# Kernel tuning notes

Hardware: AMD Instinct MI355X
Metric: run time of the kernel (lower is better)

The kernel has to match this reference:

```python
import jax, jax.numpy as jnp
import numpy as np

N, CIN, C, G, K, H, W = 2, 256, 512, 8, 3, 48, 48
CG = C // G          # channels per group (head dim) = 64
PAD = K // 2
HD, WD = H - K + 1, W - K + 1   # k/v spatial grid (pad=False convs)


def _conv(x, w, groups, pad):
    return jax.lax.conv_general_dilated(
        x, w, window_strides=(1, 1), padding=[(pad, pad), (pad, pad)],
        dimension_numbers=('NCHW', 'OIHW', 'NCHW'), feature_group_count=groups)


def setup_inputs() -> dict:
    key = jax.random.key(0)
    ks = jax.random.split(key, 32)

    def wgt(k, shape):
        fan_in = int(np.prod(shape[1:]))
        return jax.random.normal(k, shape, dtype=jnp.float32) * (fan_in ** -0.5)

    inp = {
        'x_in': jax.random.normal(ks[0], (N, CIN, H, W), dtype=jnp.float32),
        'h':    jax.random.normal(ks[1], (N, C, H, W), dtype=jnp.float32),
        'c':    jax.random.normal(ks[2], (N, C, H, W), dtype=jnp.float32),
        'tau':  jnp.full((G,), CG ** -0.5, dtype=jnp.float32),  # init (channels/groups)^-0.5
        # proj_x: 1x1 from input + intergroup 1x1 on h (groups > 1)
        'W_x':  wgt(ks[3], (C, CIN, 1, 1)),
        'W_ig': wgt(ks[4], (C, C, 1, 1)),
        # grouped KxK q/k/v projections on xh (2C channels, G groups)
        'W_q':  wgt(ks[5], (C, 2 * CG, K, K)),
        'W_k':  wgt(ks[6], (C, 2 * CG, K, K)),
        'W_v':  wgt(ks[7], (C, 2 * CG, K, K)),
    }
    for idx, gate in enumerate(['i', 'f', 'g', 'o']):
        inp[f'W{gate}_a'] = wgt(ks[8 + 3 * idx], (C, CG, 1, 1))        # grouped 1x1 on a
        inp[f'W{gate}_x'] = wgt(ks[9 + 3 * idx], (C, 2 * CG, K, K))    # grouped KxK on xh
        inp[f'b_{gate}'] = jnp.zeros((C,), dtype=jnp.float32)
    return inp


def reference(x_in, h, c, tau, W_x, W_ig, W_q, W_k, W_v,
              Wi_a, Wi_x, b_i, Wf_a, Wf_x, b_f,
              Wg_a, Wg_x, b_g, Wo_a, Wo_x, b_o):
    n = x_in.shape[0]
    # proj_x: sum of 1x1 conv branches (input + intergroup h), no bias
    x = _conv(x_in, W_x, 1, 0) + _conv(h, W_ig, 1, 0)          # [n, C, H, W]

    # xh: per-group interleave of x and h -> [n, 2C, H, W]
    xg = x.reshape(n, G, CG, H, W)
    hg = h.reshape(n, G, CG, H, W)
    xh = jnp.stack([xg, hg], axis=2).reshape(n, 2 * C, H, W)
    # dropout is identity in eval

    q = _conv(xh, W_q, G, PAD).reshape(n, G, CG, H * W)         # [n,G,Cg,Q]
    k = _conv(xh, W_k, G, 0).reshape(n, G, CG, HD * WD)         # [n,G,Cg,D]
    v = _conv(xh, W_v, G, 0).reshape(n, G, CG, HD * WD)

    logits = jnp.einsum('g,ngcq,ngcd->ngqd', tau, q, k)
    w = jax.nn.softmax(logits, axis=3)                          # [n,G,Q,D]
    a = jnp.einsum('ngcd,ngqd->ngcq', v, w).reshape(n, C, H, W)

    def gate(Wa, Wx, b):
        return _conv(a, Wa, G, 0) + _conv(xh, Wx, G, PAD) + b[None, :, None, None]

    i = jax.nn.sigmoid(gate(Wi_a, Wi_x, b_i))
    f = jax.nn.sigmoid(gate(Wf_a, Wf_x, b_f))
    g = jnp.tanh(gate(Wg_a, Wg_x, b_g))
    o = jax.nn.sigmoid(gate(Wo_a, Wo_x, b_o))

    c_new = f * c + i * g
    h_new = o * jnp.tanh(c_new)
    return h_new
```

## Files before the change

kernel.cpp:

```cpp
#include <hip/hip_runtime.h>
#include <hip/hip_bf16.h>
#include <math.h>

#define NB   2
#define CIN  256
#define CC   512
#define GG   8
#define CGR  64
#define HH   48
#define WW   48
#define PP   (HH*WW)
#define HD   46
#define WD   46
#define DD   (HD*WD)
#define DPADV 2120
#define WRT  589824

typedef __bf16 bf16x8 __attribute__((ext_vector_type(8)));
typedef float  f32x4  __attribute__((ext_vector_type(4)));

__device__ __forceinline__ bf16x8 ldb8(const __hip_bfloat16* p) {
    return *reinterpret_cast<const bf16x8*>(p);
}
__device__ __forceinline__ void store4bf(__hip_bfloat16* p, f32x4 v) {
    union { __hip_bfloat16 h[4]; uint2 u; } t;
    #pragma unroll
    for (int r = 0; r < 4; ++r) t.h[r] = (__hip_bfloat16)v[r];
    *reinterpret_cast<uint2*>(p) = t.u;
}
__device__ __forceinline__ float ex2(float x) {
    return __builtin_amdgcn_exp2f(x);
}
__device__ __forceinline__ float sig_fast(float x) {
    return __builtin_amdgcn_rcpf(1.f + ex2(-1.44269504088896f * x));
}
__device__ __forceinline__ float tanh_fast(float x) {
    return 1.f - 2.f * __builtin_amdgcn_rcpf(ex2(2.88539008177793f * x) + 1.f);
}

__global__ __launch_bounds__(256) void prep_kernel(
    const float* __restrict__ Wq, const float* __restrict__ Wk,
    const float* __restrict__ Wv, const float* __restrict__ Wix,
    const float* __restrict__ Wfx, const float* __restrict__ Wgx,
    const float* __restrict__ Wox, const float* __restrict__ Wia,
    const float* __restrict__ Wfa, const float* __restrict__ Wga,
    const float* __restrict__ Woa, const float* __restrict__ Wx,
    const float* __restrict__ Wig,
    __hip_bfloat16* __restrict__ Wr, __hip_bfloat16* __restrict__ Wa,
    __hip_bfloat16* __restrict__ Wp)
{
    const int i = blockIdx.x * 256 + threadIdx.x;
    const int N1 = 7 * WRT;
    const int N2 = N1 + 4 * 32768;
    if (i < N1) {
        const int t = i / WRT, r = i % WRT;
        const int g = r / 73728, r2 = r % 73728;
        const int chunk = r2 / 2048, r3 = r2 % 2048;
        const int och = r3 / 32, k = r3 % 32;
        const int tap = chunk >> 2;
        const int ci = (chunk & 3) * 32 + k;
        const int co = g * 64 + och;
        const float* src;
        switch (t) {
            case 0: src = Wq;  break;  case 1: src = Wk;  break;
            case 2: src = Wv;  break;  case 3: src = Wix; break;
            case 4: src = Wfx; break;  case 5: src = Wgx; break;
            default: src = Wox;
        }
        Wr[i] = (__hip_bfloat16)src[(size_t)co * 1152 + ci * 9 + tap];
    } else if (i < N2) {
        const int j = i - N1;
        const int t = j / 32768, r = j % 32768;
        const float* src = (t == 0) ? Wia : (t == 1) ? Wfa : (t == 2) ? Wga : Woa;
        Wa[j] = (__hip_bfloat16)src[r];
    } else {
        const int j = i - N2;
        const int g = j / 49152, r = j % 49152;
        const int chunk = r / 2048, r3 = r % 2048;
        const int och = r3 / 32, k = r3 % 32;
        const int c = g * 64 + och;
        const int ci = chunk * 32 + k;
        Wp[j] = (__hip_bfloat16)((ci < 256) ? Wx[(size_t)c * 256 + ci]
                                            : Wig[(size_t)c * 512 + (ci - 256)]);
    }
}

__global__ __launch_bounds__(256) void xpose_kernel(
    const float* __restrict__ x_in, const float* __restrict__ h,
    __hip_bfloat16* __restrict__ xiT, __hip_bfloat16* __restrict__ xhT)
{
    const int pt = blockIdx.x;
    const int n  = blockIdx.y;
    const int p0 = pt * 16;
    const int tid = threadIdx.x;

    __shared__ float xs[CIN * 17];
    __shared__ float hs[CC * 17];

    const float* xb = x_in + (size_t)n * CIN * PP;
    const float* hb = h + (size_t)n * CC * PP;
    #pragma unroll
    for (int k = 0; k < 16; ++k) {
        const int idx = k * 256 + tid;
        xs[(idx >> 4) * 17 + (idx & 15)] = xb[(size_t)(idx >> 4) * PP + p0 + (idx & 15)];
    }
    #pragma unroll
    for (int k = 0; k < 32; ++k) {
        const int idx = k * 256 + tid;
        hs[(idx >> 4) * 17 + (idx & 15)] = hb[(size_t)(idx >> 4) * PP + p0 + (idx & 15)];
    }
    __syncthreads();

    #pragma unroll
    for (int it = 0; it < 2; ++it) {
        const int u = it * 256 + tid;
        const int pix = u & 15, ck = u >> 4;
        union { __hip_bfloat16 h8[8]; bf16x8 v; } t;
        #pragma unroll
        for (int j = 0; j < 8; ++j)
            t.h8[j] = (__hip_bfloat16)xs[(ck * 8 + j) * 17 + pix];
        *reinterpret_cast<bf16x8*>(
            xiT + ((size_t)n * PP + p0 + pix) * 256 + ck * 8) = t.v;
    }
    #pragma unroll
    for (int it = 0; it < 4; ++it) {
        const int u = it * 256 + tid;
        const int pix = u & 15, ck = u >> 4;
        const int g = ck >> 3, c8 = (ck & 7) * 8;
        union { __hip_bfloat16 h8[8]; bf16x8 v; } t;
        #pragma unroll
        for (int j = 0; j < 8; ++j)
            t.h8[j] = (__hip_bfloat16)hs[(ck * 8 + j) * 17 + pix];
        *reinterpret_cast<bf16x8*>(
            xhT + ((size_t)(n * GG + g) * PP + p0 + pix) * 128 + 64 + c8) = t.v;
    }
}

__global__ __launch_bounds__(256) void proj_mfma_kernel(
    const __hip_bfloat16* __restrict__ xiT, const __hip_bfloat16* __restrict__ Wp,
    __hip_bfloat16* xhT)
{
    const int b = blockIdx.x;
    const int g = b & 7;
    const int j = b >> 3;
    const int n = j / 12;
    const int yt = j % 12;
    const int ng = n * GG + g;
    const int tid = threadIdx.x;
    const int w = tid >> 6, lane = tid & 63;
    const int col = lane & 15, quad = lane >> 4;
    const int y = yt * 4 + w;

    f32x4 acc[12];
    #pragma unroll
    for (int i = 0; i < 12; ++i) acc[i] = (f32x4){0.f, 0.f, 0.f, 0.f};

    const __hip_bfloat16* wgbase = Wp + (size_t)g * 24 * 2048 + col * 32 + quad * 8;

    for (int kk = 0; kk < 24; ++kk) {
        bf16x8 bfr[3];
        if (kk < 8) {
            const __hip_bfloat16* bp =
                xiT + ((size_t)n * PP + y * 48 + col) * 256 + kk * 32 + quad * 8;
            #pragma unroll
            for (int nf = 0; nf < 3; ++nf)
                bfr[nf] = ldb8(bp + (size_t)(nf * 16) * 256);
        } else {
            const int kh = kk - 8;
            const int gp = kh >> 1;
            const int c0 = (kh & 1) * 32;
            const __hip_bfloat16* bp =
                xhT + ((size_t)(n * GG + gp) * PP + y * 48 + col) * 128 + 64 + c0 + quad * 8;
            #pragma unroll
            for (int nf = 0; nf < 3; ++nf)
                bfr[nf] = ldb8(bp + (size_t)(nf * 16) * 128);
        }
        const __hip_bfloat16* wp = wgbase + kk * 2048;
        #pragma unroll
        for (int cf = 0; cf < 4; ++cf) {
            const bf16x8 af = ldb8(wp + cf * 512);
            #pragma unroll
            for (int nf = 0; nf < 3; ++nf)
                acc[cf * 3 + nf] = __builtin_amdgcn_mfma_f32_16x16x32_bf16(
                    af, bfr[nf], acc[cf * 3 + nf], 0, 0, 0);
        }
    }

    __hip_bfloat16* dst = xhT + (size_t)ng * PP * 128;
    #pragma unroll
    for (int cf = 0; cf < 4; ++cf)
        #pragma unroll
        for (int nf = 0; nf < 3; ++nf) {
            const int pix = y * 48 + nf * 16 + col;
            store4bf(dst + (size_t)pix * 128 + cf * 16 + quad * 4, acc[cf * 3 + nf]);
        }
}

__global__ __launch_bounds__(512) void conv_qkv_kernel(
    const __hip_bfloat16* __restrict__ xhT, const __hip_bfloat16* __restrict__ Wr,
    const float* __restrict__ tau,
    __hip_bfloat16* __restrict__ qT, __hip_bfloat16* __restrict__ kT,
    __hip_bfloat16* __restrict__ v)
{
    const int b = blockIdx.x;
    const int xcd = b & 7;
    const int j = b >> 3;
    const int s = xcd + 8 * (j / 12);
    const int yt = j % 12;
    const int t = s / 16;
    const int ng = s % 16;
    const int g = ng & 7;
    const int tid = threadIdx.x;
    const int w8 = tid >> 6, lane = tid & 63;
    const int yw = w8 & 3, chalf = w8 >> 2;
    const int cf0 = chalf * 2;
    const int col = lane & 15, quad = lane >> 4;
    const int y0 = yt * 4;
    const int yy = y0 + yw;
    const int ohw = (t == 0) ? 48 : 46;
    const int d0 = (t == 0) ? -1 : 0;
    const int soff = (t == 0) ? 1 : 0;
    const bool wave_active = (yy < ohw);

    __shared__ __hip_bfloat16 st[8 * 300 * 8];

    const __hip_bfloat16* slab = xhT + (size_t)ng * PP * 128;
    const __hip_bfloat16* wgbase =
        Wr + ((size_t)t * 8 + g) * 36 * 2048 + col * 32 + quad * 8;

    if (tid < 96) {
        const int ck = tid / 12, r2 = tid % 12;
        const int lr = r2 >> 1, side = r2 & 1;
        const int sc = side ? 49 : (soff ? 0 : 48);
        *reinterpret_cast<bf16x8*>(st + ((ck * 300) + lr * 50 + sc) * 8) =
            (bf16x8)(__bf16)0.f;
    }

    f32x4 acc[6];
    #pragma unroll
    for (int i = 0; i < 6; ++i) acc[i] = (f32x4){0.f, 0.f, 0.f, 0.f};

    for (int hc = 0; hc < 2; ++hc) {
        __syncthreads();
        #pragma unroll
        for (int it = 0; it < 5; ++it) {
            const int u = it * 512 + tid;
            if (u < 2304) {
                const int lr = u / 384;
                const int rem = u % 384;
                const int px = rem >> 3, ck = rem & 7;
                const int ry = y0 + d0 + lr;
                const int ryc = max(0, min(47, ry));
                bf16x8 vv = ldb8(slab + ((size_t)(ryc * 48 + px)) * 128 + hc * 64 + ck * 8);
                *reinterpret_cast<bf16x8*>(st + ((ck * 300) + lr * 50 + px + soff) * 8) =
                    (ry == ryc) ? vv : (bf16x8)(__bf16)0.f;
            }
        }
        __syncthreads();
        if (!wave_active) continue;

        #pragma unroll
        for (int ky = 0; ky < 3; ++ky) {
            const int lrk = (yw + ky) * 50;
            #pragma unroll
            for (int kx = 0; kx < 3; ++kx) {
                const int scb = col + kx;
                #pragma unroll
                for (int c32 = 0; c32 < 2; ++c32) {
                    bf16x8 bfr[3];
                    #pragma unroll
                    for (int nf = 0; nf < 3; ++nf)
                        bfr[nf] = *reinterpret_cast<const bf16x8*>(
                            st + (((c32 * 4 + quad) * 300) + lrk + nf * 16 + scb) * 8);
                    const __hip_bfloat16* wp =
                        wgbase + ((ky * 3 + kx) * 4 + hc * 2 + c32) * 2048;
                    if (t != 2) {
                        #pragma unroll
                        for (int cc = 0; cc < 2; ++cc) {
                            const bf16x8 af = ldb8(wp + (cf0 + cc) * 512);
                            #pragma unroll
                            for (int nf = 0; nf < 3; ++nf)
                                acc[cc * 3 + nf] = __builtin_amdgcn_mfma_f32_16x16x32_bf16(
                                    af, bfr[nf], acc[cc * 3 + nf], 0, 0, 0);
                        }
                    } else {
                        #pragma unroll
                        for (int cc = 0; cc < 2; ++cc) {
                            const bf16x8 af = ldb8(wp + (cf0 + cc) * 512);
                            #pragma unroll
                            for (int nf = 0; nf < 3; ++nf)
                                acc[cc * 3 + nf] = __builtin_amdgcn_mfma_f32_16x16x32_bf16(
                                    bfr[nf], af, acc[cc * 3 + nf], 0, 0, 0);
                        }
                    }
                }
            }
        }
    }

    if (!wave_active) return;
    if (t == 0) {
        const float ts = tau[g] * 1.44269504088896340736f;
        __hip_bfloat16* dst = qT + (size_t)ng * PP * 64;
        #pragma unroll
        for (int cc = 0; cc < 2; ++cc)
            #pragma unroll
            for (int nf = 0; nf < 3; ++nf) {
                const int pix = yy * 48 + nf * 16 + col;
                store4bf(dst + (size_t)pix * 64 + (cf0 + cc) * 16 + quad * 4,
                         acc[cc * 3 + nf] * ts);
            }
    } else if (t == 1) {
        __hip_bfloat16* dst = kT + (size_t)ng * DD * 64;
        #pragma unroll
        for (int cc = 0; cc < 2; ++cc)
            #pragma unroll
            for (int nf = 0; nf < 3; ++nf) {
                const int x = nf * 16 + col;
                if (x < 46) {
                    const int pix = yy * 46 + x;
                    store4bf(dst + (size_t)pix * 64 + (cf0 + cc) * 16 + quad * 4,
                             acc[cc * 3 + nf]);
                }
            }
    } else {
        __hip_bfloat16* dst = v + (size_t)ng * 64 * DPADV;
        #pragma unroll
        for (int cc = 0; cc < 2; ++cc) {
            const int co = (cf0 + cc) * 16 + col;
            #pragma unroll
            for (int nf = 0; nf < 3; ++nf) {
                const int x4 = nf * 16 + quad * 4;
                #pragma unroll
                for (int r = 0; r < 4; ++r) {
                    if (x4 + r < 46)
                        dst[(size_t)co * DPADV + yy * 46 + x4 + r] =
                            (__hip_bfloat16)acc[cc * 3 + nf][r];
                }
            }
        }
    }
}

__global__ __launch_bounds__(256) void attn_kernel(
    __hip_bfloat16* qa,
    const __hip_bfloat16* __restrict__ kT,
    const __hip_bfloat16* __restrict__ vT)
{
    const int idx = blockIdx.x;
    const int j3  = idx >> 3;
    const int sub = (j3 >= 144) ? 1 : 0;
    const int ng  = (idx & 7) + 8 * sub;
    const int qt  = j3 - 144 * sub;
    const int tid = threadIdx.x;
    const int w = tid >> 6, lane = tid & 63;
    const int col = lane & 15, quad = lane >> 4;
    const int qbase = qt * 16;

    const int it0 = w * 17;
    const int it1 = (w < 3) ? (it0 + 17) : 66;

    __shared__ float lmS[3][64];
    __shared__ float llS[3][64];
    __shared__ float laccS[3][64][16];

    __hip_bfloat16* qrow = qa + ((size_t)ng * PP + qbase + col) * CGR;
    const bf16x8 qf0 = ldb8(qrow + quad * 8);
    const bf16x8 qf1 = ldb8(qrow + 32 + quad * 8);

    const __hip_bfloat16* kbase = kT + (size_t)ng * DD * CGR;
    const __hip_bfloat16* vbase = vT + (size_t)ng * CGR * DPADV;
    const __hip_bfloat16* vrow[4];
    #pragma unroll
    for (int cf = 0; cf < 4; ++cf)
        vrow[cf] = vbase + (size_t)(cf * 16 + col) * DPADV;

    const int key0 = ((col >> 2) << 3) + (col & 3);
    const __hip_bfloat16* p0 = kbase + (size_t)(it0 * 32 + key0) * CGR + quad * 8;
    const __hip_bfloat16* p1 = p0 + 4 * CGR;

    f32x4 acc[4];
    #pragma unroll
    for (int cf = 0; cf < 4; ++cf) acc[cf] = (f32x4){0.f, 0.f, 0.f, 0.f};
    float m = -INFINITY;
    float l = 0.f;
    const f32x4 zero = {0.f, 0.f, 0.f, 0.f};

    bf16x8 A0 = ldb8(p0), A1 = ldb8(p0 + 32);
    bf16x8 B0 = ldb8(p1), B1 = ldb8(p1 + 32);

    for (int it = it0; it < it1; ++it) {
        const int dbase = it * 32;
        p0 += 32 * CGR; p1 += 32 * CGR;
        bf16x8 nA0, nA1, nB0, nB1;
        if (it + 1 < it1) {
            nA0 = ldb8(p0); nA1 = ldb8(p0 + 32);
            nB0 = ldb8(p1); nB1 = ldb8(p1 + 32);
        }

        f32x4 S0 = __builtin_amdgcn_mfma_f32_16x16x32_bf16(A0, qf0, zero, 0, 0, 0);
        S0 = __builtin_amdgcn_mfma_f32_16x16x32_bf16(A1, qf1, S0, 0, 0, 0);
        f32x4 S1 = __builtin_amdgcn_mfma_f32_16x16x32_bf16(B0, qf0, zero, 0, 0, 0);
        S1 = __builtin_amdgcn_mfma_f32_16x16x32_bf16(B1, qf1, S1, 0, 0, 0);

        const int da = dbase + quad * 8;
        const bf16x8 vf0 = ldb8(vrow[0] + da);
        const bf16x8 vf1 = ldb8(vrow[1] + da);
        const bf16x8 vf2 = ldb8(vrow[2] + da);
        const bf16x8 vf3 = ldb8(vrow[3] + da);

        const float lmx = fmaxf(fmaxf(fmaxf(S0[0], S0[1]), fmaxf(S0[2], S0[3])),
                                fmaxf(fmaxf(S1[0], S1[1]), fmaxf(S1[2], S1[3])));

        if (__any(lmx > m + 8.f)) {
            float s = lmx;
            s = fmaxf(s, __shfl_xor(s, 16, 64));
            s = fmaxf(s, __shfl_xor(s, 32, 64));
            const float mn = fmaxf(m, s);
            const float a = ex2(m - mn);
            l *= a;
            #pragma unroll
            for (int cf = 0; cf < 4; ++cf) acc[cf] *= a;
            m = mn;
        }

        float e[8];
        float lsum = 0.f;
        #pragma unroll
        for (int r = 0; r < 4; ++r) {
            e[r]     = ex2(S0[r] - m);
            e[4 + r] = ex2(S1[r] - m);
            lsum += e[r] + e[4 + r];
        }
        l += lsum;

        bf16x8 pt;
        #pragma unroll
        for (int jj = 0; jj < 8; ++jj) pt[jj] = (__bf16)e[jj];

        acc[0] = __builtin_amdgcn_mfma_f32_16x16x32_bf16(vf0, pt, acc[0], 0, 0, 0);
        acc[1] = __builtin_amdgcn_mfma_f32_16x16x32_bf16(vf1, pt, acc[1], 0, 0, 0);
        acc[2] = __builtin_amdgcn_mfma_f32_16x16x32_bf16(vf2, pt, acc[2], 0, 0, 0);
        acc[3] = __builtin_amdgcn_mfma_f32_16x16x32_bf16(vf3, pt, acc[3], 0, 0, 0);

        A0 = nA0; A1 = nA1; B0 = nB0; B1 = nB1;
    }

    if (w == 3) {
        const int dbase = 66 * 32;
        const int kk0 = min(dbase + key0, DD - 1);
        const int kk1 = min(dbase + key0 + 4, DD - 1);
        const __hip_bfloat16* t0 = kbase + (size_t)kk0 * CGR + quad * 8;
        const __hip_bfloat16* t1 = kbase + (size_t)kk1 * CGR + quad * 8;
        f32x4 S0 = __builtin_amdgcn_mfma_f32_16x16x32_bf16(ldb8(t0), qf0, zero, 0, 0, 0);
        S0 = __builtin_amdgcn_mfma_f32_16x16x32_bf16(ldb8(t0 + 32), qf1, S0, 0, 0, 0);
        f32x4 S1 = __builtin_amdgcn_mfma_f32_16x16x32_bf16(ldb8(t1), qf0, zero, 0, 0, 0);
        S1 = __builtin_amdgcn_mfma_f32_16x16x32_bf16(ldb8(t1 + 32), qf1, S1, 0, 0, 0);

        float e[8];
        #pragma unroll
        for (int r = 0; r < 4; ++r) {
            e[r]     = (dbase + quad * 8 + r     < DD) ? S0[r] : -1e30f;
            e[4 + r] = (dbase + quad * 8 + 4 + r < DD) ? S1[r] : -1e30f;
        }
        float s = fmaxf(fmaxf(fmaxf(e[0], e[1]), fmaxf(e[2], e[3])),
                        fmaxf(fmaxf(e[4], e[5]), fmaxf(e[6], e[7])));
        s = fmaxf(s, __shfl_xor(s, 16, 64));
        s = fmaxf(s, __shfl_xor(s, 32, 64));
        const float mn = fmaxf(m, s);
        const float a = ex2(m - mn);
        float lsum = 0.f;
        #pragma unroll
        for (int jj = 0; jj < 8; ++jj) { e[jj] = ex2(e[jj] - mn); lsum += e[jj]; }
        l = l * a + lsum;
        m = mn;

        bf16x8 pt;
        #pragma unroll
        for (int jj = 0; jj < 8; ++jj) pt[jj] = (__bf16)e[jj];

        int da = dbase + quad * 8;
        if (da >= DD) da = 0;
        #pragma unroll
        for (int cf = 0; cf < 4; ++cf) {
            acc[cf] *= a;
            acc[cf] = __builtin_amdgcn_mfma_f32_16x16x32_bf16(
                ldb8(vrow[cf] + da), pt, acc[cf], 0, 0, 0);
        }
    }

    if (w != 0) {
        lmS[w - 1][lane] = m;
        llS[w - 1][lane] = l;
        #pragma unroll
        for (int cf = 0; cf < 4; ++cf)
            *reinterpret_cast<f32x4*>(&laccS[w - 1][lane][cf * 4]) = acc[cf];
    }
    __syncthreads();
    if (w != 0) return;

    #pragma unroll
    for (int ww = 0; ww < 3; ++ww) {
        const float mo = lmS[ww][lane];
        const float lo = llS[ww][lane];
        const float mn = fmaxf(m, mo);
        const float a0 = ex2(m - mn);
        const float a1 = ex2(mo - mn);
        l = l * a0 + lo * a1;
        #pragma unroll
        for (int cf = 0; cf < 4; ++cf) {
            const f32x4 o = *reinterpret_cast<const f32x4*>(&laccS[ww][lane][cf * 4]);
            acc[cf] = acc[cf] * a0 + o * a1;
        }
        m = mn;
    }

    l += __shfl_xor(l, 16, 64);
    l += __shfl_xor(l, 32, 64);

    const float inv = 1.f / l;
    #pragma unroll
    for (int cf = 0; cf < 4; ++cf)
        store4bf(qrow + cf * 16 + quad * 4, acc[cf] * inv);
}

__global__ __launch_bounds__(512) void gates_kernel(
    const __hip_bfloat16* __restrict__ xhT, const __hip_bfloat16* __restrict__ aT,
    const float* __restrict__ c_in,
    const __hip_bfloat16* __restrict__ Wr, const __hip_bfloat16* __restrict__ Wa,
    const float* __restrict__ b_i, const float* __restrict__ b_f,
    const float* __restrict__ b_g, const float* __restrict__ b_o,
    float* __restrict__ h_out)
{
    const int b = blockIdx.x;
    const int xcd = b & 7;
    const int j = b >> 3;
    const int ng = xcd + 8 * (j / 48);
    const int yy = j % 48;
    const int n = ng >> 3, g = ng & 7;
    const int tid = threadIdx.x;
    const int w8 = tid >> 6, lane = tid & 63;
    const int gate = w8 & 3, chalf = w8 >> 2;
    const int cf0 = chalf * 2;
    const int col = lane & 15, quad = lane >> 4;

    __shared__ char smem[38400];
    __hip_bfloat16* st = (__hip_bfloat16*)smem;
    float* ex = (float*)smem;

    const __hip_bfloat16* slab = xhT + (size_t)ng * PP * 128;

    if (tid < 96) {
        const int ck = tid / 6, r2 = tid % 6;
        const int lr = r2 >> 1, side = r2 & 1;
        const int sc = side ? 49 : 0;
        *reinterpret_cast<bf16x8*>(st + ((ck * 150) + lr * 50 + sc) * 8) =
            (bf16x8)(__bf16)0.f;
    }
    #pragma unroll
    for (int it = 0; it < 5; ++it) {
        const int u = it * 512 + tid;
        if (u < 2304) {
            const int lr = u / 768;
            const int rem = u % 768;
            const int px = rem >> 4, ck = rem & 15;
            const int ry = yy - 1 + lr;
            const int ryc = max(0, min(47, ry));
            bf16x8 vv = ldb8(slab + ((size_t)(ryc * 48 + px)) * 128 + ck * 8);
            *reinterpret_cast<bf16x8*>(st + ((ck * 150) + lr * 50 + px + 1) * 8) =
                (ry == ryc) ? vv : (bf16x8)(__bf16)0.f;
        }
    }
    __syncthreads();

    f32x4 acc[6];
    #pragma unroll
    for (int i = 0; i < 6; ++i) acc[i] = (f32x4){0.f, 0.f, 0.f, 0.f};

    const __hip_bfloat16* wgbase =
        Wr + ((size_t)(3 + gate) * 8 + g) * 36 * 2048 + col * 32 + quad * 8;

    #pragma unroll
    for (int ky = 0; ky < 3; ++ky) {
        const int lrk = ky * 50;
        #pragma unroll
        for (int kx = 0; kx < 3; ++kx) {
            const int scb = col + kx;
            #pragma unroll
            for (int c32 = 0; c32 < 4; ++c32) {
                bf16x8 bfr[3];
                #pragma unroll
                for (int nf = 0; nf < 3; ++nf)
                    bfr[nf] = *reinterpret_cast<const bf16x8*>(
                        st + (((c32 * 4 + quad) * 150) + lrk + nf * 16 + scb) * 8);
                const __hip_bfloat16* wp =
                    wgbase + ((ky * 3 + kx) * 4 + c32) * 2048;
                #pragma unroll
                for (int cc = 0; cc < 2; ++cc) {
                    const bf16x8 af = ldb8(wp + (cf0 + cc) * 512);
                    #pragma unroll
                    for (int nf = 0; nf < 3; ++nf)
                        acc[cc * 3 + nf] = __builtin_amdgcn_mfma_f32_16x16x32_bf16(
                            af, bfr[nf], acc[cc * 3 + nf], 0, 0, 0);
                }
            }
        }
    }

    {
        const __hip_bfloat16* wa =
            Wa + (size_t)gate * 32768 + ((size_t)(g * 64) + col) * 64;
        const __hip_bfloat16* ab = aT + ((size_t)ng * PP + yy * 48) * 64;
        #pragma unroll
        for (int c32 = 0; c32 < 2; ++c32) {
            bf16x8 bfr[3];
            #pragma unroll
            for (int nf = 0; nf < 3; ++nf)
                bfr[nf] = ldb8(ab + (size_t)(nf * 16 + col) * 64 + c32 * 32 + quad * 8);
            #pragma unroll
            for (int cc = 0; cc < 2; ++cc) {
                const bf16x8 af = ldb8(wa + (size_t)((cf0 + cc) * 16) * 64 + c32 * 32 + quad * 8);
                #pragma unroll
                for (int nf = 0; nf < 3; ++nf)
                    acc[cc * 3 + nf] = __builtin_amdgcn_mfma_f32_16x16x32_bf16(
                        af, bfr[nf], acc[cc * 3 + nf], 0, 0, 0);
            }
        }
    }

    const float* bias = (gate == 0) ? b_i : (gate == 1) ? b_f : (gate == 2) ? b_g : b_o;
    #pragma unroll
    for (int cc = 0; cc < 2; ++cc) {
        #pragma unroll
        for (int r = 0; r < 4; ++r) {
            const float bv = bias[g * 64 + (cf0 + cc) * 16 + quad * 4 + r];
            #pragma unroll
            for (int nf = 0; nf < 3; ++nf)
                acc[cc * 3 + nf][r] += bv;
        }
    }

    for (int hh = 0; hh < 2; ++hh) {
        __syncthreads();
        if (chalf == hh) {
            #pragma unroll
            for (int cc = 0; cc < 2; ++cc)
                #pragma unroll
                for (int nf = 0; nf < 3; ++nf)
                    #pragma unroll
                    for (int r = 0; r < 4; ++r)
                        ex[(size_t)gate * 1536 + (cc * 16 + quad * 4 + r) * 48 + nf * 16 + col] =
                            acc[cc * 3 + nf][r];
        }
        __syncthreads();
        #pragma unroll
        for (int k2 = 0; k2 < 3; ++k2) {
            const int idx = k2 * 512 + tid;
            const int co32 = idx / 48, px = idx % 48;
            const float iv = ex[0 * 1536 + co32 * 48 + px];
            const float fv = ex[1 * 1536 + co32 * 48 + px];
            const float gv = ex[2 * 1536 + co32 * 48 + px];
            const float ov = ex[3 * 1536 + co32 * 48 + px];
            const int c = g * 64 + hh * 32 + co32;
            const size_t off = ((size_t)n * CC + c) * PP + yy * 48 + px;
            const float ig = sig_fast(iv);
            const float fg = sig_fast(fv);
            const float gg = tanh_fast(gv);
            const float og = sig_fast(ov);
            const float cn = fg * c_in[off] + ig * gg;
            h_out[off] = og * tanh_fast(cn);
        }
    }
}

extern "C" void kernel_launch(void* const* d_in, const int* in_sizes, int n_in,
                              void* d_out, int out_size, void* d_ws, size_t ws_size,
                              hipStream_t stream)
{
    const float* x_in = (const float*)d_in[0];
    const float* h    = (const float*)d_in[1];
    const float* c    = (const float*)d_in[2];
    const float* tau  = (const float*)d_in[3];
    const float* W_x  = (const float*)d_in[4];
    const float* W_ig = (const float*)d_in[5];
    const float* W_q  = (const float*)d_in[6];
    const float* W_k  = (const float*)d_in[7];
    const float* W_v  = (const float*)d_in[8];
    const float* Wi_a = (const float*)d_in[9];
    const float* Wi_x = (const float*)d_in[10];
    const float* b_i  = (const float*)d_in[11];
    const float* Wf_a = (const float*)d_in[12];
    const float* Wf_x = (const float*)d_in[13];
    const float* b_f  = (const float*)d_in[14];
    const float* Wg_a = (const float*)d_in[15];
    const float* Wg_x = (const float*)d_in[16];
    const float* b_g  = (const float*)d_in[17];
    const float* Wo_a = (const float*)d_in[18];
    const float* Wo_x = (const float*)d_in[19];
    const float* b_o  = (const float*)d_in[20];
    float* out = (float*)d_out;

    __hip_bfloat16* wsb = (__hip_bfloat16*)d_ws;
    __hip_bfloat16* xhT = wsb;
    __hip_bfloat16* qa  = xhT + (size_t)4718592;
    __hip_bfloat16* kT  = qa  + (size_t)2359296;
    __hip_bfloat16* vv  = kT  + (size_t)2166784;
    __hip_bfloat16* Wr  = vv  + (size_t)2170880;
    __hip_bfloat16* Wa  = Wr  + (size_t)4128768;
    __hip_bfloat16* Wp  = Wa  + (size_t)131072;
    __hip_bfloat16* xiT = Wp  + (size_t)393216;

    dim3 blk(256);
    dim3 blk8(512);
    prep_kernel<<<dim3(18176), blk, 0, stream>>>(
        W_q, W_k, W_v, Wi_x, Wf_x, Wg_x, Wo_x, Wi_a, Wf_a, Wg_a, Wo_a,
        W_x, W_ig, Wr, Wa, Wp);
    xpose_kernel<<<dim3(144, NB), blk, 0, stream>>>(x_in, h, xiT, xhT);
    proj_mfma_kernel<<<dim3(192), blk, 0, stream>>>(xiT, Wp, xhT);
    conv_qkv_kernel<<<dim3(576), blk8, 0, stream>>>(xhT, Wr, tau, qa, kT, vv);
    attn_kernel<<<dim3(2304), blk, 0, stream>>>(qa, kT, vv);
    gates_kernel<<<dim3(768), blk8, 0, stream>>>(
        xhT, qa, c, Wr, Wa, b_i, b_f, b_g, b_o, out);
}
```

Measured before the change: 324.8 us.

## Process four query tiles per attention block to reuse K/V loads

Each attention block now handles 64 queries (four 16-row tiles) instead of 16, so every K and V fragment loaded from memory feeds four tiles' MFMAs. The grid shrinks from 2304 to 576 blocks, and the cross-wave softmax merge becomes a two-level tree reduction through a shared buffer. The aim is to cut global/L2 traffic for K and V. In exchange, register pressure rises with 16 accumulators per thread, the K register prefetch is dropped, and fewer blocks are available to hide latency.

```diff
diff --git a/kernel.cpp b/kernel.cpp
--- a/kernel.cpp
+++ b/kernel.cpp
@@ -349,24 +349,27 @@
 {
     const int idx = blockIdx.x;
     const int j3  = idx >> 3;
-    const int sub = (j3 >= 144) ? 1 : 0;
+    const int sub = (j3 >= 36) ? 1 : 0;
     const int ng  = (idx & 7) + 8 * sub;
-    const int qt  = j3 - 144 * sub;
+    const int qt  = j3 - 36 * sub;
     const int tid = threadIdx.x;
     const int w = tid >> 6, lane = tid & 63;
     const int col = lane & 15, quad = lane >> 4;
-    const int qbase = qt * 16;
+    const int qbase = qt * 64;
 
     const int it0 = w * 17;
     const int it1 = (w < 3) ? (it0 + 17) : 66;
 
-    __shared__ float lmS[3][64];
-    __shared__ float llS[3][64];
-    __shared__ float laccS[3][64][16];
-
-    __hip_bfloat16* qrow = qa + ((size_t)ng * PP + qbase + col) * CGR;
-    const bf16x8 qf0 = ldb8(qrow + quad * 8);
-    const bf16x8 qf1 = ldb8(qrow + 32 + quad * 8);
+    __shared__ float mg[2][4][64][20];
+
+    __hip_bfloat16* qrow[4];
+    bf16x8 qf0[4], qf1[4];
+    #pragma unroll
+    for (int t = 0; t < 4; ++t) {
+        qrow[t] = qa + ((size_t)ng * PP + qbase + t * 16 + col) * CGR;
+        qf0[t] = ldb8(qrow[t] + quad * 8);
+        qf1[t] = ldb8(qrow[t] + 32 + quad * 8);
+    }
 
     const __hip_bfloat16* kbase = kT + (size_t)ng * DD * CGR;
     const __hip_bfloat16* vbase = vT + (size_t)ng * CGR * DPADV;
@@ -379,29 +382,21 @@
     const __hip_bfloat16* p0 = kbase + (size_t)(it0 * 32 + key0) * CGR + quad * 8;
     const __hip_bfloat16* p1 = p0 + 4 * CGR;
 
-    f32x4 acc[4];
-    #pragma unroll
-    for (int cf = 0; cf < 4; ++cf) acc[cf] = (f32x4){0.f, 0.f, 0.f, 0.f};
-    float m = -INFINITY;
-    float l = 0.f;
+    f32x4 acc[4][4];
+    #pragma unroll
+    for (int t = 0; t < 4; ++t)
+        #pragma unroll
+        for (int cf = 0; cf < 4; ++cf)
+            acc[t][cf] = (f32x4){0.f, 0.f, 0.f, 0.f};
+    float m[4] = {-INFINITY, -INFINITY, -INFINITY, -INFINITY};
+    float l[4] = {0.f, 0.f, 0.f, 0.f};
     const f32x4 zero = {0.f, 0.f, 0.f, 0.f};
-
-    bf16x8 A0 = ldb8(p0), A1 = ldb8(p0 + 32);
-    bf16x8 B0 = ldb8(p1), B1 = ldb8(p1 + 32);
 
     for (int it = it0; it < it1; ++it) {
         const int dbase = it * 32;
+        const bf16x8 K0a = ldb8(p0), K0b = ldb8(p0 + 32);
+        const bf16x8 K1a = ldb8(p1), K1b = ldb8(p1 + 32);
         p0 += 32 * CGR; p1 += 32 * CGR;
-        bf16x8 nA0, nA1, nB0, nB1;
-        if (it + 1 < it1) {
-            nA0 = ldb8(p0); nA1 = ldb8(p0 + 32);
-            nB0 = ldb8(p1); nB1 = ldb8(p1 + 32);
-        }
-
-        f32x4 S0 = __builtin_amdgcn_mfma_f32_16x16x32_bf16(A0, qf0, zero, 0, 0, 0);
-        S0 = __builtin_amdgcn_mfma_f32_16x16x32_bf16(A1, qf1, S0, 0, 0, 0);
-        f32x4 S1 = __builtin_amdgcn_mfma_f32_16x16x32_bf16(B0, qf0, zero, 0, 0, 0);
-        S1 = __builtin_amdgcn_mfma_f32_16x16x32_bf16(B1, qf1, S1, 0, 0, 0);
 
         const int da = dbase + quad * 8;
         const bf16x8 vf0 = ldb8(vrow[0] + da);
@@ -409,119 +404,171 @@
         const bf16x8 vf2 = ldb8(vrow[2] + da);
         const bf16x8 vf3 = ldb8(vrow[3] + da);
 
-        const float lmx = fmaxf(fmaxf(fmaxf(S0[0], S0[1]), fmaxf(S0[2], S0[3])),
-                                fmaxf(fmaxf(S1[0], S1[1]), fmaxf(S1[2], S1[3])));
-
-        if (__any(lmx > m + 8.f)) {
-            float s = lmx;
-            s = fmaxf(s, __shfl_xor(s, 16, 64));
-            s = fmaxf(s, __shfl_xor(s, 32, 64));
-            const float mn = fmaxf(m, s);
-            const float a = ex2(m - mn);
-            l *= a;
-            #pragma unroll
-            for (int cf = 0; cf < 4; ++cf) acc[cf] *= a;
-            m = mn;
-        }
-
-        float e[8];
-        float lsum = 0.f;
-        #pragma unroll
-        for (int r = 0; r < 4; ++r) {
-            e[r]     = ex2(S0[r] - m);
-            e[4 + r] = ex2(S1[r] - m);
-            lsum += e[r] + e[4 + r];
-        }
-        l += lsum;
-
-        bf16x8 pt;
-        #pragma unroll
-        for (int jj = 0; jj < 8; ++jj) pt[jj] = (__bf16)e[jj];
-
-        acc[0] = __builtin_amdgcn_mfma_f32_16x16x32_bf16(vf0, pt, acc[0], 0, 0, 0);
-        acc[1] = __builtin_amdgcn_mfma_f32_16x16x32_bf16(vf1, pt, acc[1], 0, 0, 0);
-        acc[2] = __builtin_amdgcn_mfma_f32_16x16x32_bf16(vf2, pt, acc[2], 0, 0, 0);
-        acc[3] = __builtin_amdgcn_mfma_f32_16x16x32_bf16(vf3, pt, acc[3], 0, 0, 0);
-
-        A0 = nA0; A1 = nA1; B0 = nB0; B1 = nB1;
+        #pragma unroll
+        for (int t = 0; t < 4; ++t) {
+            f32x4 S0 = __builtin_amdgcn_mfma_f32_16x16x32_bf16(K0a, qf0[t], zero, 0, 0, 0);
+            S0 = __builtin_amdgcn_mfma_f32_16x16x32_bf16(K0b, qf1[t], S0, 0, 0, 0);
+            f32x4 S1 = __builtin_amdgcn_mfma_f32_16x16x32_bf16(K1a, qf0[t], zero, 0, 0, 0);
+            S1 = __builtin_amdgcn_mfma_f32_16x16x32_bf16(K1b, qf1[t], S1, 0, 0, 0);
+
+            const float lmx = fmaxf(fmaxf(fmaxf(S0[0], S0[1]), fmaxf(S0[2], S0[3])),
+                                    fmaxf(fmaxf(S1[0], S1[1]), fmaxf(S1[2], S1[3])));
+            if (__any(lmx > m[t] + 8.f)) {
+                float s = lmx;
+                s = fmaxf(s, __shfl_xor(s, 16, 64));
+                s = fmaxf(s, __shfl_xor(s, 32, 64));
+                const float mn = fmaxf(m[t], s);
+                const float a = ex2(m[t] - mn);
+                l[t] *= a;
+                #pragma unroll
+                for (int cf = 0; cf < 4; ++cf) acc[t][cf] *= a;
+                m[t] = mn;
+            }
+
+            float e[8];
+            float lsum = 0.f;
+            #pragma unroll
+            for (int r = 0; r < 4; ++r) {
+                e[r]     = ex2(S0[r] - m[t]);
+                e[4 + r] = ex2(S1[r] - m[t]);
+                lsum += e[r] + e[4 + r];
+            }
+            l[t] += lsum;
+
+            bf16x8 pt;
+            #pragma unroll
+            for (int jj = 0; jj < 8; ++jj) pt[jj] = (__bf16)e[jj];
+
+            acc[t][0] = __builtin_amdgcn_mfma_f32_16x16x32_bf16(vf0, pt, acc[t][0], 0, 0, 0);
+            acc[t][1] = __builtin_amdgcn_mfma_f32_16x16x32_bf16(vf1, pt, acc[t][1], 0, 0, 0);
+            acc[t][2] = __builtin_amdgcn_mfma_f32_16x16x32_bf16(vf2, pt, acc[t][2], 0, 0, 0);
+            acc[t][3] = __builtin_amdgcn_mfma_f32_16x16x32_bf16(vf3, pt, acc[t][3], 0, 0, 0);
+        }
     }
 
     if (w == 3) {
         const int dbase = 66 * 32;
         const int kk0 = min(dbase + key0, DD - 1);
         const int kk1 = min(dbase + key0 + 4, DD - 1);
-        const __hip_bfloat16* t0 = kbase + (size_t)kk0 * CGR + quad * 8;
-        const __hip_bfloat16* t1 = kbase + (size_t)kk1 * CGR + quad * 8;
-        f32x4 S0 = __builtin_amdgcn_mfma_f32_16x16x32_bf16(ldb8(t0), qf0, zero, 0, 0, 0);
-        S0 = __builtin_amdgcn_mfma_f32_16x16x32_bf16(ldb8(t0 + 32), qf1, S0, 0, 0, 0);
-        f32x4 S1 = __builtin_amdgcn_mfma_f32_16x16x32_bf16(ldb8(t1), qf0, zero, 0, 0, 0);
-        S1 = __builtin_amdgcn_mfma_f32_16x16x32_bf16(ldb8(t1 + 32), qf1, S1, 0, 0, 0);
-
-        float e[8];
-        #pragma unroll
-        for (int r = 0; r < 4; ++r) {
-            e[r]     = (dbase + quad * 8 + r     < DD) ? S0[r] : -1e30f;
-            e[4 + r] = (dbase + quad * 8 + 4 + r < DD) ? S1[r] : -1e30f;
-        }
-        float s = fmaxf(fmaxf(fmaxf(e[0], e[1]), fmaxf(e[2], e[3])),
-                        fmaxf(fmaxf(e[4], e[5]), fmaxf(e[6], e[7])));
-        s = fmaxf(s, __shfl_xor(s, 16, 64));
-        s = fmaxf(s, __shfl_xor(s, 32, 64));
-        const float mn = fmaxf(m, s);
-        const float a = ex2(m - mn);
-        float lsum = 0.f;
-        #pragma unroll
-        for (int jj = 0; jj < 8; ++jj) { e[jj] = ex2(e[jj] - mn); lsum += e[jj]; }
-        l = l * a + lsum;
-        m = mn;
-
-        bf16x8 pt;
-        #pragma unroll
-        for (int jj = 0; jj < 8; ++jj) pt[jj] = (__bf16)e[jj];
+        const __hip_bfloat16* t0p = kbase + (size_t)kk0 * CGR + quad * 8;
+        const __hip_bfloat16* t1p = kbase + (size_t)kk1 * CGR + quad * 8;
+        const bf16x8 Ka = ldb8(t0p), Kb = ldb8(t0p + 32);
+        const bf16x8 Kc = ldb8(t1p), Kd = ldb8(t1p + 32);
 
         int da = dbase + quad * 8;
         if (da >= DD) da = 0;
-        #pragma unroll
-        for (int cf = 0; cf < 4; ++cf) {
-            acc[cf] *= a;
-            acc[cf] = __builtin_amdgcn_mfma_f32_16x16x32_bf16(
-                ldb8(vrow[cf] + da), pt, acc[cf], 0, 0, 0);
-        }
-    }
-
-    if (w != 0) {
-        lmS[w - 1][lane] = m;
-        llS[w - 1][lane] = l;
-        #pragma unroll
-        for (int cf = 0; cf < 4; ++cf)
-            *reinterpret_cast<f32x4*>(&laccS[w - 1][lane][cf * 4]) = acc[cf];
+        const bf16x8 tv0 = ldb8(vrow[0] + da);
+        const bf16x8 tv1 = ldb8(vrow[1] + da);
+        const bf16x8 tv2 = ldb8(vrow[2] + da);
+        const bf16x8 tv3 = ldb8(vrow[3] + da);
+
+        #pragma unroll
+        for (int t = 0; t < 4; ++t) {
+            f32x4 S0 = __builtin_amdgcn_mfma_f32_16x16x32_bf16(Ka, qf0[t], zero, 0, 0, 0);
+            S0 = __builtin_amdgcn_mfma_f32_16x16x32_bf16(Kb, qf1[t], S0, 0, 0, 0);
+            f32x4 S1 = __builtin_amdgcn_mfma_f32_16x16x32_bf16(Kc, qf0[t], zero, 0, 0, 0);
+            S1 = __builtin_amdgcn_mfma_f32_16x16x32_bf16(Kd, qf1[t], S1, 0, 0, 0);
+
+            float e[8];
+            #pragma unroll
+            for (int r = 0; r < 4; ++r) {
+                e[r]     = (dbase + quad * 8 + r     < DD) ? S0[r] : -1e30f;
+                e[4 + r] = (dbase + quad * 8 + 4 + r < DD) ? S1[r] : -1e30f;
+            }
+            float s = fmaxf(fmaxf(fmaxf(e[0], e[1]), fmaxf(e[2], e[3])),
+                            fmaxf(fmaxf(e[4], e[5]), fmaxf(e[6], e[7])));
+            s = fmaxf(s, __shfl_xor(s, 16, 64));
+            s = fmaxf(s, __shfl_xor(s, 32, 64));
+            const float mn = fmaxf(m[t], s);
+            const float a = ex2(m[t] - mn);
+            float lsum = 0.f;
+            #pragma unroll
+            for (int jj = 0; jj < 8; ++jj) { e[jj] = ex2(e[jj] - mn); lsum += e[jj]; }
+            l[t] = l[t] * a + lsum;
+            m[t] = mn;
+
+            bf16x8 pt;
+            #pragma unroll
+            for (int jj = 0; jj < 8; ++jj) pt[jj] = (__bf16)e[jj];
+
+            #pragma unroll
+            for (int cf = 0; cf < 4; ++cf) acc[t][cf] *= a;
+            acc[t][0] = __builtin_amdgcn_mfma_f32_16x16x32_bf16(tv0, pt, acc[t][0], 0, 0, 0);
+            acc[t][1] = __builtin_amdgcn_mfma_f32_16x16x32_bf16(tv1, pt, acc[t][1], 0, 0, 0);
+            acc[t][2] = __builtin_amdgcn_mfma_f32_16x16x32_bf16(tv2, pt, acc[t][2], 0, 0, 0);
+            acc[t][3] = __builtin_amdgcn_mfma_f32_16x16x32_bf16(tv3, pt, acc[t][3], 0, 0, 0);
+        }
+    }
+
+    if (w == 1 || w == 3) {
+        const int bs = (w == 3) ? 1 : 0;
+        #pragma unroll
+        for (int t = 0; t < 4; ++t) {
+            #pragma unroll
+            for (int cf = 0; cf < 4; ++cf)
+                *reinterpret_cast<f32x4*>(&mg[bs][t][lane][cf * 4]) = acc[t][cf];
+            mg[bs][t][lane][16] = m[t];
+            mg[bs][t][lane][17] = l[t];
+        }
+    }
+    __syncthreads();
+    if (w == 0 || w == 2) {
+        const int bs = (w == 2) ? 1 : 0;
+        #pragma unroll
+        for (int t = 0; t < 4; ++t) {
+            const float mo = mg[bs][t][lane][16];
+            const float lo = mg[bs][t][lane][17];
+            const float mn = fmaxf(m[t], mo);
+            const float a0 = ex2(m[t] - mn);
+            const float a1 = ex2(mo - mn);
+            l[t] = l[t] * a0 + lo * a1;
+            #pragma unroll
+            for (int cf = 0; cf < 4; ++cf) {
+                const f32x4 o = *reinterpret_cast<const f32x4*>(&mg[bs][t][lane][cf * 4]);
+                acc[t][cf] = acc[t][cf] * a0 + o * a1;
+            }
+            m[t] = mn;
+        }
+    }
+    __syncthreads();
+    if (w == 2) {
+        #pragma unroll
+        for (int t = 0; t < 4; ++t) {
+            #pragma unroll
+            for (int cf = 0; cf < 4; ++cf)
+                *reinterpret_cast<f32x4*>(&mg[0][t][lane][cf * 4]) = acc[t][cf];
+            mg[0][t][lane][16] = m[t];
+            mg[0][t][lane][17] = l[t];
+        }
     }
     __syncthreads();
     if (w != 0) return;
 
     #pragma unroll
-    for (int ww = 0; ww < 3; ++ww) {
-        const float mo = lmS[ww][lane];
-        const float lo = llS[ww][lane];
-        const float mn = fmaxf(m, mo);
-        const float a0 = ex2(m - mn);
+    for (int t = 0; t < 4; ++t) {
+        const float mo = mg[0][t][lane][16];
+        const float lo = mg[0][t][lane][17];
+        const float mn = fmaxf(m[t], mo);
+        const float a0 = ex2(m[t] - mn);
         const float a1 = ex2(mo - mn);
-        l = l * a0 + lo * a1;
+        l[t] = l[t] * a0 + lo * a1;
         #pragma unroll
         for (int cf = 0; cf < 4; ++cf) {
-            const f32x4 o = *reinterpret_cast<const f32x4*>(&laccS[ww][lane][cf * 4]);
-            acc[cf] = acc[cf] * a0 + o * a1;
-        }
-        m = mn;
-    }
-
-    l += __shfl_xor(l, 16, 64);
-    l += __shfl_xor(l, 32, 64);
-
-    const float inv = 1.f / l;
-    #pragma unroll
-    for (int cf = 0; cf < 4; ++cf)
-        store4bf(qrow + cf * 16 + quad * 4, acc[cf] * inv);
+            const f32x4 o = *reinterpret_cast<const f32x4*>(&mg[0][t][lane][cf * 4]);
+            acc[t][cf] = acc[t][cf] * a0 + o * a1;
+        }
+        m[t] = mn;
+    }
+
+    #pragma unroll
+    for (int t = 0; t < 4; ++t) {
+        l[t] += __shfl_xor(l[t], 16, 64);
+        l[t] += __shfl_xor(l[t], 32, 64);
+        const float inv = 1.f / l[t];
+        #pragma unroll
+        for (int cf = 0; cf < 4; ++cf)
+            store4bf(qrow[t] + cf * 16 + quad * 4, acc[t][cf] * inv);
+    }
 }
 
 __global__ __launch_bounds__(512) void gates_kernel(
@@ -718,7 +765,7 @@
     xpose_kernel<<<dim3(144, NB), blk, 0, stream>>>(x_in, h, xiT, xhT);
     proj_mfma_kernel<<<dim3(192), blk, 0, stream>>>(xiT, Wp, xhT);
     conv_qkv_kernel<<<dim3(576), blk8, 0, stream>>>(xhT, Wr, tau, qa, kT, vv);
-    attn_kernel<<<dim3(2304), blk, 0, stream>>>(qa, kT, vv);
+    attn_kernel<<<dim3(576), blk, 0, stream>>>(qa, kT, vv);
     gates_kernel<<<dim3(768), blk8, 0, stream>>>(
         xhT, qa, c, Wr, Wa, b_i, b_f, b_g, b_o, out);
 }
```

Result: faster. 271.8 us (-16.3%).
